# Kernel optimization log

Hardware: AMD Instinct MI355X
Metric: run time of the kernel (lower is better)

The kernel has to match this reference:

```python
import jax, jax.numpy as jnp
import numpy as np

B, T, C = 2, 2048, 1024
H = 16
D = C // H  # head_dim = 64


def setup_inputs() -> dict:
    key = jax.random.key(0)
    k1, k2, k3, k4, k5 = jax.random.split(key, 5)
    s = 1.0 / np.sqrt(C)
    return {
        "x": jax.random.normal(k1, (B, T, C), dtype=jnp.float32),
        "w_qkv": jax.random.normal(k2, (C, 3 * C), dtype=jnp.float32) * s,
        "b_qkv": jax.random.normal(k3, (3 * C,), dtype=jnp.float32) * 0.01,
        "w_out": jax.random.normal(k4, (C, C), dtype=jnp.float32) * s,
        "b_out": jax.random.normal(k5, (C,), dtype=jnp.float32) * 0.01,
    }


def reference(x, w_qkv, b_qkv, w_out, b_out):
    Bx, Tx, Cx = x.shape
    qkv = x @ w_qkv + b_qkv                      # [B,T,3C]
    qkv = qkv.reshape(Bx, Tx, 3, H, D)
    q, k, v = qkv[:, :, 0], qkv[:, :, 1], qkv[:, :, 2]  # [B,T,H,D]
    # [B,H,T,T] scores with scaling
    scores = jnp.einsum("bqhd,bkhd->bhqk", q, k) / np.sqrt(D).astype(np.float32)
    causal = jnp.tril(jnp.ones((Tx, Tx), dtype=bool))
    scores = jnp.where(causal[None, None], scores, -jnp.inf)
    attn = jax.nn.softmax(scores, axis=-1)
    out = jnp.einsum("bhqk,bkhd->bqhd", attn, v).reshape(Bx, Tx, Cx)
    return out @ w_out + b_out
```

## Files before the change

### kernel.cpp

```cpp
#include <hip/hip_runtime.h>
#include <stdint.h>

typedef unsigned short u16;
typedef __attribute__((ext_vector_type(8))) short bfrag;
typedef __attribute__((ext_vector_type(4))) short bfrag4;
typedef __attribute__((ext_vector_type(4))) float f32x4;

#define MFMA_BF16 __builtin_amdgcn_mfma_f32_16x16x32_bf16

static constexpr int Bc = 2;
static constexpr int Tc = 2048;
static constexpr int Cc = 1024;
static constexpr int Hc = 16;
static constexpr int Dc = 64;
static constexpr int N3 = 3 * Cc;

__device__ __forceinline__ u16 f2bf(float f) {
    union { unsigned int i; float f; } v; v.f = f;
    unsigned int u = v.i;
    u += 0x7fffu + ((u >> 16) & 1u);
    return (u16)(u >> 16);
}
__device__ __forceinline__ unsigned int fbits(float f) {
    union { unsigned int i; float f; } v; v.f = f; return v.i;
}
__device__ __forceinline__ unsigned int pack_bf2(float hi, float lo) {
    return __builtin_amdgcn_perm(fbits(hi), fbits(lo), 0x07060302u);
}

#if __has_builtin(__builtin_amdgcn_mfma_f32_16x16x16bf16_1k)
__device__ __forceinline__ f32x4 MFMA16(bfrag4 a, bfrag4 b, f32x4 c) {
    return __builtin_amdgcn_mfma_f32_16x16x16bf16_1k(a, b, c, 0, 0, 0);
}
#elif __has_builtin(__builtin_amdgcn_mfma_f32_16x16x16_bf16)
__device__ __forceinline__ f32x4 MFMA16(bfrag4 a, bfrag4 b, f32x4 c) {
    return __builtin_amdgcn_mfma_f32_16x16x16_bf16(a, b, c, 0, 0, 0);
}
#else
__device__ __forceinline__ f32x4 MFMA16(bfrag4 a, bfrag4 b, f32x4 c) {
    bfrag a8 = {a[0], a[1], a[2], a[3], 0, 0, 0, 0};
    bfrag b8 = {b[0], b[1], b[2], b[3], 0, 0, 0, 0};
    return MFMA_BF16(a8, b8, c, 0, 0, 0);
}
#endif

__device__ __forceinline__ void async_load16(const u16* g, u16* lds) {
    __builtin_amdgcn_global_load_lds(
        (const __attribute__((address_space(1))) unsigned int*)g,
        (__attribute__((address_space(3))) unsigned int*)lds, 16, 0, 0);
}

__global__ __launch_bounds__(256) void prep(
    const float* __restrict__ x, const float* __restrict__ w_qkv,
    const float* __restrict__ w_out, u16* __restrict__ xb,
    u16* __restrict__ WqkvT, u16* __restrict__ WoutT) {
    __shared__ u16 tile[32][33];
    const int blk = blockIdx.x, tid = threadIdx.x;
    if (blk < 4096) {
        const int i = (blk * 256 + tid) * 4;
        const float4 v = *(const float4*)(x + i);
        ushort4 o;
        o.x = f2bf(v.x); o.y = f2bf(v.y); o.z = f2bf(v.z); o.w = f2bf(v.w);
        *(ushort4*)(xb + i) = o;
        return;
    }
    const int tx = tid & 31, ty = tid >> 5;
    const float* in; u16* out; int rows, cols, c0, r0;
    if (blk < 4096 + 3072) {
        const int t = blk - 4096;
        in = w_qkv; out = WqkvT; rows = 1024; cols = 3072;
        c0 = (t % 96) * 32; r0 = (t / 96) * 32;
    } else {
        const int t = blk - 7168;
        in = w_out; out = WoutT; rows = 1024; cols = 1024;
        c0 = (t & 31) * 32; r0 = (t >> 5) * 32;
    }
    for (int i = 0; i < 4; i++)
        tile[ty + 8 * i][tx] = f2bf(in[(size_t)(r0 + ty + 8 * i) * cols + c0 + tx]);
    __syncthreads();
    for (int i = 0; i < 4; i++)
        out[(size_t)(c0 + ty + 8 * i) * rows + r0 + tx] = tile[tx][ty + 8 * i];
}

__global__ void transpose_v(const u16* __restrict__ P, u16* __restrict__ Vt) {
    __shared__ u16 tile[32][33];
    const int bh = blockIdx.z, b = bh >> 4, h = bh & 15;
    const int t0 = blockIdx.x * 32, d0 = blockIdx.y * 32;
    const int tx = threadIdx.x, ty = threadIdx.y;
    const u16* src = P + (size_t)b * Tc * N3 + 2 * Cc + h * Dc;
    for (int i = 0; i < 4; i++)
        tile[ty + 8 * i][tx] = src[(size_t)(t0 + ty + 8 * i) * N3 + d0 + tx];
    __syncthreads();
    u16* dst = Vt + ((size_t)bh * Dc) * Tc;
    for (int i = 0; i < 4; i++)
        dst[(size_t)(d0 + ty + 8 * i) * Tc + t0 + tx] = tile[tx][ty + 8 * i];
}

template <int MODE>
__global__ __launch_bounds__(256) void gemm_bt(
    const u16* __restrict__ A, const u16* __restrict__ BT,
    const float* __restrict__ bias, void* __restrict__ out_p,
    int M, int Nn, int K) {
    __shared__ __align__(16) u16 As[2][128 * 32];
    __shared__ __align__(16) u16 Bs[2][128 * 32];

    const int tid  = threadIdx.x;
    const int wave = tid >> 6, lane = tid & 63;
    const int quad = lane >> 4, l16 = lane & 15;
    const int wm = wave & 1, wn = wave >> 1;
    const int m0 = blockIdx.y * 128, n0 = blockIdx.x * 128;

    f32x4 acc[4][4];
    #pragma unroll
    for (int i = 0; i < 4; i++)
        #pragma unroll
        for (int j = 0; j < 4; j++)
            acc[i][j] = (f32x4){0.f, 0.f, 0.f, 0.f};

    const int rloc = 2 * (lane >> 3) + ((lane >> 2) & 1);
    const int cg   = ((lane & 3) ^ ((lane >> 3) & 3)) * 8;
    const int rk   = (l16 >> 1) & 3;
    const int rodd = (l16 & 1) * 32;

    const int T = K >> 5;
    #define STAGE(t, bsel)                                                      \
        {                                                                       \
            const int k0_ = (t) << 5;                                           \
            _Pragma("unroll")                                                   \
            for (int j = 0; j < 2; j++) {                                       \
                const int R0 = wave * 32 + j * 16;                              \
                async_load16(A  + (size_t)(m0 + R0 + rloc) * K + k0_ + cg,      \
                             &As[bsel][R0 * 32]);                               \
                async_load16(BT + (size_t)(n0 + R0 + rloc) * K + k0_ + cg,      \
                             &Bs[bsel][R0 * 32]);                               \
            }                                                                   \
        }

    STAGE(0, 0);
    for (int t = 0; t < T; t++) {
        __syncthreads();
        if (t + 1 < T) STAGE(t + 1, (t + 1) & 1);
        const u16* Ab = As[t & 1];
        const u16* Bb = Bs[t & 1];
        bfrag af[4], bf[4];
        #pragma unroll
        for (int mt = 0; mt < 4; mt++) {
            const int r = wm * 64 + mt * 16 + l16;
            af[mt] = *(const bfrag*)(Ab + (r >> 1) * 64 + rodd + (quad ^ rk) * 8);
        }
        #pragma unroll
        for (int nt = 0; nt < 4; nt++) {
            const int r = wn * 64 + nt * 16 + l16;
            bf[nt] = *(const bfrag*)(Bb + (r >> 1) * 64 + rodd + (quad ^ rk) * 8);
        }
        #pragma unroll
        for (int mt = 0; mt < 4; mt++)
            #pragma unroll
            for (int nt = 0; nt < 4; nt++)
                acc[mt][nt] = MFMA_BF16(af[mt], bf[nt], acc[mt][nt], 0, 0, 0);
    }
    #undef STAGE

    #pragma unroll
    for (int nt = 0; nt < 4; nt++) {
        const int gn = n0 + wn * 64 + nt * 16 + l16;
        const float bv = bias[gn];
        #pragma unroll
        for (int mt = 0; mt < 4; mt++) {
            #pragma unroll
            for (int r = 0; r < 4; r++) {
                const int gm = m0 + wm * 64 + mt * 16 + quad * 4 + r;
                if (MODE == 1)
                    ((u16*)out_p)[(size_t)gm * Nn + gn] = f2bf(acc[mt][nt][r] + bv);
                else
                    ((float*)out_p)[(size_t)gm * Nn + gn] = acc[mt][nt][r] + bv;
            }
        }
    }
}

__global__ __launch_bounds__(256, 4) void attn_kernel(
    const u16* __restrict__ QKVp, const u16* __restrict__ Vt,
    u16* __restrict__ Ob) {
    __shared__ __align__(16) u16 KsF[2][64 * 64];
    __shared__ __align__(16) u16 VsF[2][64 * 64];

    const int tid  = threadIdx.x;
    const int wave = tid >> 6, lane = tid & 63;
    const int quad = lane >> 4, l16 = lane & 15;

    const int bh = blockIdx.x & 31;
    const int jq = 31 - (blockIdx.x >> 5);
    const int b = bh >> 4, h = bh & 15;
    const u16* Qp = QKVp + (size_t)b * Tc * N3 + h * Dc;
    const u16* Kp = Qp + Cc;
    const u16* Vp = Vt + (size_t)bh * Dc * Tc;

    const int qw = jq * 64 + wave * 16;

    const int row8 = lane >> 3;
    const int swz  = ((lane & 7) ^ row8) * 8;
    const int pk0 = ((quad)     ^ (l16 & 7)) * 8;
    const int pk1 = ((quad + 4) ^ (l16 & 7)) * 8;

    bfrag qf0, qf1;
    {
        const u16* qp = Qp + (size_t)(qw + l16) * N3 + quad * 8;
        qf0 = *(const bfrag*)qp;
        qf1 = *(const bfrag*)(qp + 32);
    }

    float l_i = 0.f;
    f32x4 oacc[4];
    #pragma unroll
    for (int g = 0; g < 4; g++) oacc[g] = (f32x4){0.f, 0.f, 0.f, 0.f};

    #define STAGEKV(t, bsel)                                                    \
        {                                                                       \
            const int k0_ = (t) * 64;                                           \
            _Pragma("unroll")                                                   \
            for (int j = 0; j < 2; j++) {                                       \
                const int rr = wave * 16 + j * 8;                               \
                const int gr = rr + row8;                                       \
                async_load16(Kp + (size_t)(k0_ + gr) * N3 + swz,                \
                             &KsF[bsel][rr * 64]);                              \
                async_load16(Vp + (size_t)gr * Tc + k0_ + swz,                  \
                             &VsF[bsel][rr * 64]);                              \
            }                                                                   \
        }

    STAGEKV(0, 0);
    for (int t = 0; t <= jq; t++) {
        __syncthreads();
        if (t < jq) STAGEKV(t + 1, (t + 1) & 1);
        const u16* Kb = KsF[t & 1];
        const u16* Vb = VsF[t & 1];
        const int k0 = t * 64;
        (void)k0;

        f32x4 s[4];
        #pragma unroll
        for (int g = 0; g < 4; g++) {
            const u16* kb = Kb + (g * 16 + l16) * 64;
            bfrag kf0 = *(const bfrag*)(kb + pk0);
            bfrag kf1 = *(const bfrag*)(kb + pk1);
            f32x4 z = (f32x4){0.f, 0.f, 0.f, 0.f};
            z = MFMA_BF16(kf0, qf0, z, 0, 0, 0);
            z = MFMA_BF16(kf1, qf1, z, 0, 0, 0);
            s[g] = z;
        }

        #pragma unroll
        for (int g = 0; g < 4; g++)
            #pragma unroll
            for (int r = 0; r < 4; r++)
                s[g][r] = __expf(s[g][r] * 0.125f);
        if (t == jq) {
            #pragma unroll
            for (int g = 0; g < 4; g++)
                #pragma unroll
                for (int r = 0; r < 4; r++)
                    if (g * 16 + quad * 4 + r > wave * 16 + l16) s[g][r] = 0.f;
        }
        #pragma unroll
        for (int g = 0; g < 4; g++)
            l_i += s[g][0] + s[g][1] + s[g][2] + s[g][3];

        #pragma unroll
        for (int g = 0; g < 4; g++) {
            union { unsigned int u[2]; bfrag4 v; } pf;
            pf.u[0] = pack_bf2(s[g][1], s[g][0]);
            pf.u[1] = pack_bf2(s[g][3], s[g][2]);
            const int vc = ((2 * g + (quad >> 1)) ^ (l16 & 7)) * 8 + (quad & 1) * 4;
            #pragma unroll
            for (int ng = 0; ng < 4; ng++) {
                const bfrag4 vf = *(const bfrag4*)(Vb + (ng * 16 + l16) * 64 + vc);
                oacc[ng] = MFMA16(vf, pf.v, oacc[ng]);
            }
        }
    }
    #undef STAGEKV

    float rs = l_i;
    rs += __shfl_xor(rs, 16);
    rs += __shfl_xor(rs, 32);
    const float inv = 1.f / rs;
    const int q = qw + l16;
    u16* orow = Ob + (size_t)(b * Tc + q) * Cc + h * Dc + quad * 4;
    #pragma unroll
    for (int ng = 0; ng < 4; ng++) {
        ushort4 o;
        o.x = f2bf(oacc[ng][0] * inv);
        o.y = f2bf(oacc[ng][1] * inv);
        o.z = f2bf(oacc[ng][2] * inv);
        o.w = f2bf(oacc[ng][3] * inv);
        *(ushort4*)(orow + ng * 16) = o;
    }
}

extern "C" void kernel_launch(void* const* d_in, const int* in_sizes, int n_in,
                              void* d_out, int out_size, void* d_ws, size_t ws_size,
                              hipStream_t stream) {
    const float* x     = (const float*)d_in[0];
    const float* w_qkv = (const float*)d_in[1];
    const float* b_qkv = (const float*)d_in[2];
    const float* w_out = (const float*)d_in[3];
    const float* b_out = (const float*)d_in[4];
    float* out = (float*)d_out;
    u16* ws  = (u16*)d_ws;

    u16* xb    = ws;
    u16* WqkvT = xb    + (size_t)4096 * 1024;
    u16* WoutT = WqkvT + (size_t)3072 * 1024;
    u16* QKVp  = WoutT + (size_t)1024 * 1024;
    u16* Vt    = QKVp  + (size_t)4096 * 3072;
    u16* Ao    = xb;

    prep<<<8192, 256, 0, stream>>>(x, w_qkv, w_out, xb, WqkvT, WoutT);
    gemm_bt<1><<<dim3(3072 / 128, 4096 / 128), 256, 0, stream>>>(
        xb, WqkvT, b_qkv, QKVp, 4096, 3072, 1024);
    transpose_v<<<dim3(Tc / 32, Dc / 32, Bc * Hc), dim3(32, 8), 0, stream>>>(
        QKVp, Vt);
    attn_kernel<<<1024, 256, 0, stream>>>(QKVp, Vt, Ao);
    gemm_bt<0><<<dim3(1024 / 128, 4096 / 128), 256, 0, stream>>>(
        Ao, WoutT, b_out, out, 4096, 1024, 1024);
}
```

Baseline: 182.6 us.

## Fuse V transpose into QKV GEMM epilogue via shared-memory staging

Removes the separate transpose_v kernel. The QKV GEMM now writes Q and K into a narrower [T,2C] buffer, and for V column tiles it stages the bf16 results transposed in shared memory, then writes them directly to the Vt layout with 16-byte stores. This saves one kernel launch and a full read/write pass over V. The cost is a larger shared-memory allocation for MODE 1 (128x136 elements) and extra barriers in the epilogue, which could lower occupancy of the QKV GEMM.

```diff
diff --git a/kernel.cpp b/kernel.cpp
--- a/kernel.cpp
+++ b/kernel.cpp
@@ -13,7 +13,7 @@
 static constexpr int Cc = 1024;
 static constexpr int Hc = 16;
 static constexpr int Dc = 64;
-static constexpr int N3 = 3 * Cc;
+static constexpr int N2 = 2 * Cc;
 
 __device__ __forceinline__ u16 f2bf(float f) {
     union { unsigned int i; float f; } v; v.f = f;
@@ -82,27 +82,13 @@
         out[(size_t)(c0 + ty + 8 * i) * rows + r0 + tx] = tile[tx][ty + 8 * i];
 }
 
-__global__ void transpose_v(const u16* __restrict__ P, u16* __restrict__ Vt) {
-    __shared__ u16 tile[32][33];
-    const int bh = blockIdx.z, b = bh >> 4, h = bh & 15;
-    const int t0 = blockIdx.x * 32, d0 = blockIdx.y * 32;
-    const int tx = threadIdx.x, ty = threadIdx.y;
-    const u16* src = P + (size_t)b * Tc * N3 + 2 * Cc + h * Dc;
-    for (int i = 0; i < 4; i++)
-        tile[ty + 8 * i][tx] = src[(size_t)(t0 + ty + 8 * i) * N3 + d0 + tx];
-    __syncthreads();
-    u16* dst = Vt + ((size_t)bh * Dc) * Tc;
-    for (int i = 0; i < 4; i++)
-        dst[(size_t)(d0 + ty + 8 * i) * Tc + t0 + tx] = tile[tx][ty + 8 * i];
-}
-
 template <int MODE>
 __global__ __launch_bounds__(256) void gemm_bt(
     const u16* __restrict__ A, const u16* __restrict__ BT,
     const float* __restrict__ bias, void* __restrict__ out_p,
-    int M, int Nn, int K) {
-    __shared__ __align__(16) u16 As[2][128 * 32];
-    __shared__ __align__(16) u16 Bs[2][128 * 32];
+    u16* __restrict__ Vt, int M, int Nn, int K) {
+    constexpr int SELEMS = (MODE == 1) ? 128 * 136 : 4 * 4096;
+    __shared__ __align__(16) u16 smem[SELEMS];
 
     const int tid  = threadIdx.x;
     const int wave = tid >> 6, lane = tid & 63;
@@ -126,13 +112,14 @@
     #define STAGE(t, bsel)                                                      \
         {                                                                       \
             const int k0_ = (t) << 5;                                           \
+            const int ao_ = (bsel) * 4096;                                      \
             _Pragma("unroll")                                                   \
             for (int j = 0; j < 2; j++) {                                       \
                 const int R0 = wave * 32 + j * 16;                              \
                 async_load16(A  + (size_t)(m0 + R0 + rloc) * K + k0_ + cg,      \
-                             &As[bsel][R0 * 32]);                               \
+                             smem + ao_ + R0 * 32);                             \
                 async_load16(BT + (size_t)(n0 + R0 + rloc) * K + k0_ + cg,      \
-                             &Bs[bsel][R0 * 32]);                               \
+                             smem + 8192 + ao_ + R0 * 32);                      \
             }                                                                   \
         }
 
@@ -140,8 +127,8 @@
     for (int t = 0; t < T; t++) {
         __syncthreads();
         if (t + 1 < T) STAGE(t + 1, (t + 1) & 1);
-        const u16* Ab = As[t & 1];
-        const u16* Bb = Bs[t & 1];
+        const u16* Ab = smem + (t & 1) * 4096;
+        const u16* Bb = smem + 8192 + (t & 1) * 4096;
         bfrag af[4], bf[4];
         #pragma unroll
         for (int mt = 0; mt < 4; mt++) {
@@ -161,26 +148,54 @@
     }
     #undef STAGE
 
-    #pragma unroll
-    for (int nt = 0; nt < 4; nt++) {
-        const int gn = n0 + wn * 64 + nt * 16 + l16;
-        const float bv = bias[gn];
-        #pragma unroll
-        for (int mt = 0; mt < 4; mt++) {
-            #pragma unroll
-            for (int r = 0; r < 4; r++) {
-                const int gm = m0 + wm * 64 + mt * 16 + quad * 4 + r;
-                if (MODE == 1)
-                    ((u16*)out_p)[(size_t)gm * Nn + gn] = f2bf(acc[mt][nt][r] + bv);
-                else
-                    ((float*)out_p)[(size_t)gm * Nn + gn] = acc[mt][nt][r] + bv;
+    if (MODE == 1 && n0 >= 2048) {
+        __syncthreads();
+        #pragma unroll
+        for (int nt = 0; nt < 4; nt++) {
+            const int ln = wn * 64 + nt * 16 + l16;
+            const float bv = bias[n0 + ln];
+            u16* col = smem + ln * 136;
+            #pragma unroll
+            for (int mt = 0; mt < 4; mt++) {
+                const int lmb = wm * 64 + mt * 16 + quad * 4;
+                #pragma unroll
+                for (int r = 0; r < 4; r++)
+                    col[lmb + r] = f2bf(acc[mt][nt][r] + bv);
             }
         }
+        __syncthreads();
+        const int bb = m0 >> 11, t0 = m0 & 2047;
+        const int h0 = (n0 - 2048) >> 6;
+        const int dl = tid >> 1;
+        const int th = (tid & 1) * 64;
+        u16* dst = Vt + ((size_t)(bb * Hc + h0 + (dl >> 6)) * Dc + (dl & 63)) * Tc
+                      + t0 + th;
+        const u16* srcr = smem + dl * 136 + th;
+        #pragma unroll
+        for (int c = 0; c < 8; c++)
+            *(uint4*)(dst + c * 8) = *(const uint4*)(srcr + c * 8);
+    } else {
+        #pragma unroll
+        for (int nt = 0; nt < 4; nt++) {
+            const int gn = n0 + wn * 64 + nt * 16 + l16;
+            const float bv = bias[gn];
+            #pragma unroll
+            for (int mt = 0; mt < 4; mt++) {
+                #pragma unroll
+                for (int r = 0; r < 4; r++) {
+                    const int gm = m0 + wm * 64 + mt * 16 + quad * 4 + r;
+                    if (MODE == 1)
+                        ((u16*)out_p)[(size_t)gm * Nn + gn] = f2bf(acc[mt][nt][r] + bv);
+                    else
+                        ((float*)out_p)[(size_t)gm * Nn + gn] = acc[mt][nt][r] + bv;
+                }
+            }
+        }
     }
 }
 
 __global__ __launch_bounds__(256, 4) void attn_kernel(
-    const u16* __restrict__ QKVp, const u16* __restrict__ Vt,
+    const u16* __restrict__ QKp, const u16* __restrict__ Vt,
     u16* __restrict__ Ob) {
     __shared__ __align__(16) u16 KsF[2][64 * 64];
     __shared__ __align__(16) u16 VsF[2][64 * 64];
@@ -192,7 +207,7 @@
     const int bh = blockIdx.x & 31;
     const int jq = 31 - (blockIdx.x >> 5);
     const int b = bh >> 4, h = bh & 15;
-    const u16* Qp = QKVp + (size_t)b * Tc * N3 + h * Dc;
+    const u16* Qp = QKp + (size_t)b * Tc * N2 + h * Dc;
     const u16* Kp = Qp + Cc;
     const u16* Vp = Vt + (size_t)bh * Dc * Tc;
 
@@ -205,7 +220,7 @@
 
     bfrag qf0, qf1;
     {
-        const u16* qp = Qp + (size_t)(qw + l16) * N3 + quad * 8;
+        const u16* qp = Qp + (size_t)(qw + l16) * N2 + quad * 8;
         qf0 = *(const bfrag*)qp;
         qf1 = *(const bfrag*)(qp + 32);
     }
@@ -222,7 +237,7 @@
             for (int j = 0; j < 2; j++) {                                       \
                 const int rr = wave * 16 + j * 8;                               \
                 const int gr = rr + row8;                                       \
-                async_load16(Kp + (size_t)(k0_ + gr) * N3 + swz,                \
+                async_load16(Kp + (size_t)(k0_ + gr) * N2 + swz,                \
                              &KsF[bsel][rr * 64]);                              \
                 async_load16(Vp + (size_t)gr * Tc + k0_ + swz,                  \
                              &VsF[bsel][rr * 64]);                              \
@@ -235,8 +250,6 @@
         if (t < jq) STAGEKV(t + 1, (t + 1) & 1);
         const u16* Kb = KsF[t & 1];
         const u16* Vb = VsF[t & 1];
-        const int k0 = t * 64;
-        (void)k0;
 
         f32x4 s[4];
         #pragma unroll
@@ -312,16 +325,14 @@
     u16* xb    = ws;
     u16* WqkvT = xb    + (size_t)4096 * 1024;
     u16* WoutT = WqkvT + (size_t)3072 * 1024;
-    u16* QKVp  = WoutT + (size_t)1024 * 1024;
-    u16* Vt    = QKVp  + (size_t)4096 * 3072;
+    u16* QKp   = WoutT + (size_t)1024 * 1024;
+    u16* Vt    = QKp   + (size_t)4096 * 2048;
     u16* Ao    = xb;
 
     prep<<<8192, 256, 0, stream>>>(x, w_qkv, w_out, xb, WqkvT, WoutT);
     gemm_bt<1><<<dim3(3072 / 128, 4096 / 128), 256, 0, stream>>>(
-        xb, WqkvT, b_qkv, QKVp, 4096, 3072, 1024);
-    transpose_v<<<dim3(Tc / 32, Dc / 32, Bc * Hc), dim3(32, 8), 0, stream>>>(
-        QKVp, Vt);
-    attn_kernel<<<1024, 256, 0, stream>>>(QKVp, Vt, Ao);
+        xb, WqkvT, b_qkv, QKp, Vt, 4096, 2048, 1024);
+    attn_kernel<<<1024, 256, 0, stream>>>(QKp, Vt, Ao);
     gemm_bt<0><<<dim3(1024 / 128, 4096 / 128), 256, 0, stream>>>(
-        Ao, WoutT, b_out, out, 4096, 1024, 1024);
-}
+        Ao, WoutT, b_out, out, nullptr, 4096, 1024, 1024);
+}
```

Result: no change. 182.9 us (+0.2%).
